# Performance work log

Measured on AMD Instinct MI355X. Metric: run time of the kernel, lower is better.

The kernel has to match this reference:

```python
import jax, jax.numpy as jnp
import numpy as np


def setup_inputs() -> dict:
    key = jax.random.key(0)
    ks = jax.random.split(key, 8)
    B, S, F, K, E, N = 20000, 10, 128, 16, 128, 200000
    nodes = jax.random.randint(ks[0], (B,), 0, N)
    neigh_idx = jax.random.randint(ks[1], (B, S), 0, N)
    self_table = jax.random.normal(ks[2], (N, F), dtype=jnp.float32)
    neigh_table = jax.random.normal(ks[3], (N, F), dtype=jnp.float32)
    center = jax.random.normal(ks[4], (K, F), dtype=jnp.float32)
    cluster_mask = jax.random.uniform(ks[5], (K, F), dtype=jnp.float32)
    # xavier-like scaling keeps exp(relu(.)) in a sane range
    weight = jax.random.normal(ks[6], (E, 2 * F), dtype=jnp.float32) * 0.05
    alpha = jax.random.normal(ks[7], (2 * F, 1), dtype=jnp.float32) * 0.05
    return {"nodes": nodes, "neigh_idx": neigh_idx, "self_table": self_table,
            "neigh_table": neigh_table, "center": center, "cluster_mask": cluster_mask,
            "weight": weight, "alpha": alpha}


def reference(nodes, neigh_idx, self_table, neigh_table, center, cluster_mask, weight, alpha):
    B, S = neigh_idx.shape
    F = self_table.shape[1]
    self_feat = self_table[nodes]                       # (B, F)
    neigh = neigh_table[neigh_idx]                      # (B, S, F) gather (== mask.matmul in original)
    # attention over sampled neighbors: exp(relu([self || neigh] @ alpha))
    a_self, a_neigh = alpha[:F, 0], alpha[F:, 0]        # split cat-matmul
    logits = self_feat @ a_self                         # (B,)
    logits = logits[:, None] + neigh @ a_neigh          # (B, S)
    att = jnp.exp(jax.nn.relu(logits))
    att_norm = att / jnp.sum(att, axis=1, keepdims=True)
    # inverse-distance soft assignment to k centers (Student-t, degree 1)
    n2 = jnp.sum(neigh * neigh, axis=-1)                # (B, S)
    c2 = jnp.sum(center * center, axis=-1)              # (K,)
    cross = jnp.einsum('bsf,kf->bsk', neigh, center)    # (B, S, K)
    q = 1.0 / (n2[:, :, None] - 2.0 * cross + c2[None, None, :] + 1.0)  # (B, S, K)
    # clustered features: sum_k q[b,s,k] * mask[k,f] * neigh[b,s,f]
    clustered = neigh * jnp.einsum('bsk,kf->bsf', q, cluster_mask)      # (B, S, F)
    neigh_agg = jnp.sum(clustered * att_norm[:, :, None], axis=1)       # (B, F)
    combined = jnp.concatenate([self_feat, neigh_agg], axis=1)          # (B, 2F)
    return jax.nn.relu(combined @ weight.T)                             # (B, E)
```

## Files before the change

kernel.cpp:

```cpp
#include <hip/hip_runtime.h>
#include <hip/hip_bf16.h>

typedef unsigned short ushort_t;
typedef __attribute__((ext_vector_type(4))) float v4f;
typedef __attribute__((ext_vector_type(8))) short v8s;

#define FDIM 128
#define KCLUST 16
#define CSTRIDE 264

__device__ __forceinline__ ushort_t f2bf(float x) {
    unsigned int u = __float_as_uint(x);
    unsigned int r = (u + 0x7fffu + ((u >> 16) & 1u)) >> 16;
    return (ushort_t)r;
}

__device__ __forceinline__ float wave_reduce_sum(float v) {
    #pragma unroll
    for (int off = 32; off > 0; off >>= 1) v += __shfl_xor(v, off, 64);
    return v;
}

__global__ void pack_weight(const float* __restrict__ W, ushort_t* __restrict__ Wb,
                            long total, long valid) {
    long i = ((long)blockIdx.x * blockDim.x + threadIdx.x) * 4;
    if (i >= total) return;
    float4 v;
    if (i < valid) v = *(const float4*)(W + i);
    else           v = make_float4(0.f, 0.f, 0.f, 0.f);
    ushort_t* dst = Wb + i;
    dst[0] = f2bf(v.x); dst[1] = f2bf(v.y); dst[2] = f2bf(v.z); dst[3] = f2bf(v.w);
}

__global__ __launch_bounds__(256) void fused_agg(
    const int* __restrict__ nodes, const int* __restrict__ neigh_idx,
    const float* __restrict__ self_table, const float* __restrict__ neigh_table,
    const float* __restrict__ center, const float* __restrict__ cluster_mask,
    const float* __restrict__ alpha, const ushort_t* __restrict__ Wb,
    float* __restrict__ out, int B, int S, int E) {

    __shared__ __align__(16) ushort_t comb[16 * CSTRIDE];
    __shared__ __align__(16) float nbuf[4 * 144];
    __shared__ __align__(16) float qbuf[4 * 16];

    int t = threadIdx.x;
    int lane = t & 63, wave = t >> 6;
    int l16 = lane & 15, quad = lane >> 4;

    for (int i = t; i < (12 * CSTRIDE) / 2; i += 256)
        ((unsigned*)(comb + 4 * CSTRIDE))[i] = 0u;

    float as0 = alpha[lane],       as1 = alpha[lane + 64];
    float an0 = alpha[128 + lane], an1 = alpha[192 + lane];

    float cc[32];
    {
        const float* cb = center + l16 * FDIM + quad * 32;
        #pragma unroll
        for (int j = 0; j < 32; j += 4) {
            float4 v = *(const float4*)(cb + j);
            cc[j] = v.x; cc[j+1] = v.y; cc[j+2] = v.z; cc[j+3] = v.w;
        }
    }
    float mk0[KCLUST], mk1[KCLUST];
    #pragma unroll
    for (int kk = 0; kk < KCLUST; kk++) {
        mk0[kk] = cluster_mask[kk * FDIM + lane];
        mk1[kk] = cluster_mask[kk * FDIM + 64 + lane];
    }

    int b0 = blockIdx.x * 4;
    int b = b0 + wave;
    float* nb = nbuf + wave * 144;
    float* qb = qbuf + wave * 16;
    ushort_t* crow = comb + wave * CSTRIDE;

    if (b < B) {
        size_t node = (size_t)nodes[b];
        float s0 = self_table[node * FDIM + lane];
        float s1 = self_table[node * FDIM + 64 + lane];
        float ls = wave_reduce_sum(s0 * as0 + s1 * as1);

        float acc0 = 0.f, acc1 = 0.f, attsum = 0.f;
        const int* nidx = neigh_idx + (size_t)b * S;
        size_t g = (size_t)nidx[0];
        float n0 = neigh_table[g * FDIM + lane];
        float n1 = neigh_table[g * FDIM + 64 + lane];
        for (int s = 0; s < S; s++) {
            float cn0 = n0, cn1 = n1;
            if (s + 1 < S) {
                g = (size_t)nidx[s + 1];
                n0 = neigh_table[g * FDIM + lane];
                n1 = neigh_table[g * FDIM + 64 + lane];
            }
            float ln = wave_reduce_sum(cn0 * an0 + cn1 * an1);
            float att = __expf(fmaxf(ls + ln, 0.f));
            nb[lane + (lane >> 5) * 4] = cn0;
            int f2 = lane + 64;
            nb[f2 + (f2 >> 5) * 4] = cn1;
            float d = 0.f;
            const float* nbb = nb + quad * 36;
            #pragma unroll
            for (int i = 0; i < 8; i++) {
                float4 f4 = *(const float4*)(nbb + i * 4);
                float t0 = f4.x - cc[i*4+0]; d = fmaf(t0, t0, d);
                float t1 = f4.y - cc[i*4+1]; d = fmaf(t1, t1, d);
                float t2 = f4.z - cc[i*4+2]; d = fmaf(t2, t2, d);
                float t3 = f4.w - cc[i*4+3]; d = fmaf(t3, t3, d);
            }
            d += __shfl_xor(d, 16, 64);
            d += __shfl_xor(d, 32, 64);
            float q = __fdividef(att, d + 1.0f);
            if (lane < 16) qb[lane] = q;
            float4 q0 = *(const float4*)(qb + 0);
            float4 q1 = *(const float4*)(qb + 4);
            float4 q2 = *(const float4*)(qb + 8);
            float4 q3 = *(const float4*)(qb + 12);
            float m0, m1;
            m0  = q0.x*mk0[0]  + q0.y*mk0[1]  + q0.z*mk0[2]  + q0.w*mk0[3];
            m0 += q1.x*mk0[4]  + q1.y*mk0[5]  + q1.z*mk0[6]  + q1.w*mk0[7];
            m0 += q2.x*mk0[8]  + q2.y*mk0[9]  + q2.z*mk0[10] + q2.w*mk0[11];
            m0 += q3.x*mk0[12] + q3.y*mk0[13] + q3.z*mk0[14] + q3.w*mk0[15];
            m1  = q0.x*mk1[0]  + q0.y*mk1[1]  + q0.z*mk1[2]  + q0.w*mk1[3];
            m1 += q1.x*mk1[4]  + q1.y*mk1[5]  + q1.z*mk1[6]  + q1.w*mk1[7];
            m1 += q2.x*mk1[8]  + q2.y*mk1[9]  + q2.z*mk1[10] + q2.w*mk1[11];
            m1 += q3.x*mk1[12] + q3.y*mk1[13] + q3.z*mk1[14] + q3.w*mk1[15];
            acc0 += cn0 * m0;
            acc1 += cn1 * m1;
            attsum += att;
        }
        float inv = __fdividef(1.0f, attsum);
        crow[lane]       = f2bf(s0);
        crow[lane + 64]  = f2bf(s1);
        crow[lane + 128] = f2bf(acc0 * inv);
        crow[lane + 192] = f2bf(acc1 * inv);
    } else {
        crow[lane] = 0; crow[lane + 64] = 0;
        crow[lane + 128] = 0; crow[lane + 192] = 0;
    }
    __syncthreads();

    v8s afr[8];
    #pragma unroll
    for (int kk = 0; kk < 8; kk++)
        afr[kk] = *(const v8s*)(comb + l16 * CSTRIDE + kk * 32 + quad * 8);

    int Ntiles = (E + 15) >> 4;
    for (int nt = wave; nt < Ntiles; nt += 4) {
        const ushort_t* wrow = Wb + ((size_t)(nt * 16 + l16)) * 256 + quad * 8;
        v4f acc = {0.f, 0.f, 0.f, 0.f};
        #pragma unroll
        for (int kk = 0; kk < 8; kk++) {
            v8s bfr = *(const v8s*)(wrow + kk * 32);
            acc = __builtin_amdgcn_mfma_f32_16x16x32_bf16(afr[kk], bfr, acc, 0, 0, 0);
        }
        int gcol = nt * 16 + l16;
        if (gcol < E) {
            #pragma unroll
            for (int rr = 0; rr < 4; rr++) {
                int r16 = quad * 4 + rr;
                if (r16 < 4) {
                    int grow = b0 + r16;
                    if (grow < B)
                        out[(size_t)grow * E + gcol] = fmaxf(acc[rr], 0.f);
                }
            }
        }
    }
}

extern "C" void kernel_launch(void* const* d_in, const int* in_sizes, int n_in,
                              void* d_out, int out_size, void* d_ws, size_t ws_size,
                              hipStream_t stream) {
    const int*   nodes        = (const int*)d_in[0];
    const int*   neigh_idx    = (const int*)d_in[1];
    const float* self_table   = (const float*)d_in[2];
    const float* neigh_table  = (const float*)d_in[3];
    const float* center       = (const float*)d_in[4];
    const float* cluster_mask = (const float*)d_in[5];
    const float* weight       = (const float*)d_in[6];
    const float* alpha        = (const float*)d_in[7];
    float* out = (float*)d_out;

    int B = in_sizes[0];
    int S = in_sizes[1] / B;
    int E = in_sizes[6] / (2 * FDIM);

    int Np = ((E + 15) / 16) * 16;
    ushort_t* Wb = (ushort_t*)d_ws;

    long totalW = (long)Np * 256;
    long validW = (long)E * 256;
    int blksW = (int)((totalW + 1023) / 1024);
    pack_weight<<<blksW, 256, 0, stream>>>(weight, Wb, totalW, validW);

    int nblk = (B + 3) / 4;
    fused_agg<<<nblk, 256, 0, stream>>>(
        nodes, neigh_idx, self_table, neigh_table, center, cluster_mask, alpha,
        Wb, out, B, S, E);
}
```

Before: 285.2 us.

## Compute neighbor attention, distances and cluster mixing with bf16 MFMA per wave

Each wave now stages its 10 neighbor rows as bf16 in shared memory, zero-padded to 16. It then uses MFMA to compute the neighbor-center cross terms, the neighbor norms and the attention logits, and a second MFMA pass to multiply the soft-assignment matrix by the transposed cluster mask. This replaces the serial per-neighbor loop of wave reductions and scalar FMAs. The cost is bf16 rounding inside the distance and attention math (norm minus cross terms can lose precision), more shared memory and a per-block setup of converted center and mask tables.

```diff
diff --git a/kernel.cpp b/kernel.cpp
--- a/kernel.cpp
+++ b/kernel.cpp
@@ -8,6 +8,8 @@
 #define FDIM 128
 #define KCLUST 16
 #define CSTRIDE 264
+#define NSTRIDE 136
+#define QSTRIDE 40
 
 __device__ __forceinline__ ushort_t f2bf(float x) {
     unsigned int u = __float_as_uint(x);
@@ -40,110 +42,152 @@
     float* __restrict__ out, int B, int S, int E) {
 
     __shared__ __align__(16) ushort_t comb[16 * CSTRIDE];
-    __shared__ __align__(16) float nbuf[4 * 144];
-    __shared__ __align__(16) float qbuf[4 * 16];
+    __shared__ __align__(16) ushort_t nrow[4][16 * NSTRIDE];
+    __shared__ __align__(16) ushort_t cenB[16 * NSTRIDE];
+    __shared__ __align__(16) ushort_t maskT[FDIM * QSTRIDE];
+    __shared__ __align__(16) ushort_t aB[FDIM];
+    __shared__ __align__(16) ushort_t qmat[4][16 * QSTRIDE];
+    __shared__ __align__(16) float    n2w[4][16];
+    __shared__ __align__(16) float    c2s[KCLUST];
 
     int t = threadIdx.x;
     int lane = t & 63, wave = t >> 6;
     int l16 = lane & 15, quad = lane >> 4;
 
+    for (int i = t; i < KCLUST * FDIM; i += 256) {
+        int k = i >> 7, f = i & 127;
+        cenB[k * NSTRIDE + f] = f2bf(center[i]);
+        maskT[f * QSTRIDE + k] = f2bf(cluster_mask[i]);
+    }
+    for (int i = t; i < FDIM * 12; i += 256) {
+        int f = i / 12, c = i - f * 12;
+        ((unsigned*)maskT)[f * (QSTRIDE / 2) + 8 + c] = 0u;
+    }
+    if (t < FDIM) aB[t] = f2bf(alpha[128 + t]);
+    if (t < KCLUST) {
+        const float4* cp = (const float4*)(center + t * FDIM);
+        float acc = 0.f;
+        #pragma unroll
+        for (int j = 0; j < 32; j++) {
+            float4 v = cp[j];
+            acc += v.x * v.x + v.y * v.y + v.z * v.z + v.w * v.w;
+        }
+        c2s[t] = acc;
+    }
     for (int i = t; i < (12 * CSTRIDE) / 2; i += 256)
         ((unsigned*)(comb + 4 * CSTRIDE))[i] = 0u;
-
-    float as0 = alpha[lane],       as1 = alpha[lane + 64];
-    float an0 = alpha[128 + lane], an1 = alpha[192 + lane];
-
-    float cc[32];
     {
-        const float* cb = center + l16 * FDIM + quad * 32;
-        #pragma unroll
-        for (int j = 0; j < 32; j += 4) {
-            float4 v = *(const float4*)(cb + j);
-            cc[j] = v.x; cc[j+1] = v.y; cc[j+2] = v.z; cc[j+3] = v.w;
-        }
-    }
-    float mk0[KCLUST], mk1[KCLUST];
-    #pragma unroll
-    for (int kk = 0; kk < KCLUST; kk++) {
-        mk0[kk] = cluster_mask[kk * FDIM + lane];
-        mk1[kk] = cluster_mask[kk * FDIM + 64 + lane];
+        unsigned* qz = (unsigned*)(qmat[wave]);
+        #pragma unroll
+        for (int j = 0; j < 2; j++) {
+            int d = lane + 64 * j;
+            int r = d >> 3, c = d & 7;
+            qz[r * (QSTRIDE / 2) + 8 + c] = 0u;
+        }
     }
 
     int b0 = blockIdx.x * 4;
     int b = b0 + wave;
-    float* nb = nbuf + wave * 144;
-    float* qb = qbuf + wave * 16;
+    ushort_t* nr = nrow[wave];
+    ushort_t* qm = qmat[wave];
+    float* n2p = n2w[wave];
     ushort_t* crow = comb + wave * CSTRIDE;
 
+    float ls = 0.f;
     if (b < B) {
         size_t node = (size_t)nodes[b];
         float s0 = self_table[node * FDIM + lane];
         float s1 = self_table[node * FDIM + 64 + lane];
-        float ls = wave_reduce_sum(s0 * as0 + s1 * as1);
-
-        float acc0 = 0.f, acc1 = 0.f, attsum = 0.f;
+        float as0 = alpha[lane], as1 = alpha[lane + 64];
+        ls = wave_reduce_sum(s0 * as0 + s1 * as1);
+        crow[lane] = f2bf(s0);
+        crow[64 + lane] = f2bf(s1);
         const int* nidx = neigh_idx + (size_t)b * S;
-        size_t g = (size_t)nidx[0];
-        float n0 = neigh_table[g * FDIM + lane];
-        float n1 = neigh_table[g * FDIM + 64 + lane];
         for (int s = 0; s < S; s++) {
-            float cn0 = n0, cn1 = n1;
-            if (s + 1 < S) {
-                g = (size_t)nidx[s + 1];
-                n0 = neigh_table[g * FDIM + lane];
-                n1 = neigh_table[g * FDIM + 64 + lane];
-            }
-            float ln = wave_reduce_sum(cn0 * an0 + cn1 * an1);
-            float att = __expf(fmaxf(ls + ln, 0.f));
-            nb[lane + (lane >> 5) * 4] = cn0;
-            int f2 = lane + 64;
-            nb[f2 + (f2 >> 5) * 4] = cn1;
-            float d = 0.f;
-            const float* nbb = nb + quad * 36;
-            #pragma unroll
-            for (int i = 0; i < 8; i++) {
-                float4 f4 = *(const float4*)(nbb + i * 4);
-                float t0 = f4.x - cc[i*4+0]; d = fmaf(t0, t0, d);
-                float t1 = f4.y - cc[i*4+1]; d = fmaf(t1, t1, d);
-                float t2 = f4.z - cc[i*4+2]; d = fmaf(t2, t2, d);
-                float t3 = f4.w - cc[i*4+3]; d = fmaf(t3, t3, d);
-            }
-            d += __shfl_xor(d, 16, 64);
-            d += __shfl_xor(d, 32, 64);
-            float q = __fdividef(att, d + 1.0f);
-            if (lane < 16) qb[lane] = q;
-            float4 q0 = *(const float4*)(qb + 0);
-            float4 q1 = *(const float4*)(qb + 4);
-            float4 q2 = *(const float4*)(qb + 8);
-            float4 q3 = *(const float4*)(qb + 12);
-            float m0, m1;
-            m0  = q0.x*mk0[0]  + q0.y*mk0[1]  + q0.z*mk0[2]  + q0.w*mk0[3];
-            m0 += q1.x*mk0[4]  + q1.y*mk0[5]  + q1.z*mk0[6]  + q1.w*mk0[7];
-            m0 += q2.x*mk0[8]  + q2.y*mk0[9]  + q2.z*mk0[10] + q2.w*mk0[11];
-            m0 += q3.x*mk0[12] + q3.y*mk0[13] + q3.z*mk0[14] + q3.w*mk0[15];
-            m1  = q0.x*mk1[0]  + q0.y*mk1[1]  + q0.z*mk1[2]  + q0.w*mk1[3];
-            m1 += q1.x*mk1[4]  + q1.y*mk1[5]  + q1.z*mk1[6]  + q1.w*mk1[7];
-            m1 += q2.x*mk1[8]  + q2.y*mk1[9]  + q2.z*mk1[10] + q2.w*mk1[11];
-            m1 += q3.x*mk1[12] + q3.y*mk1[13] + q3.z*mk1[14] + q3.w*mk1[15];
-            acc0 += cn0 * m0;
-            acc1 += cn1 * m1;
-            attsum += att;
-        }
-        float inv = __fdividef(1.0f, attsum);
-        crow[lane]       = f2bf(s0);
-        crow[lane + 64]  = f2bf(s1);
-        crow[lane + 128] = f2bf(acc0 * inv);
-        crow[lane + 192] = f2bf(acc1 * inv);
+            size_t g = (size_t)nidx[s];
+            float2 v = *(const float2*)(neigh_table + g * FDIM + 2 * lane);
+            unsigned pk = ((unsigned)f2bf(v.y) << 16) | (unsigned)f2bf(v.x);
+            *(unsigned*)(nr + s * NSTRIDE + 2 * lane) = pk;
+        }
+        for (int s = S; s < 16; s++)
+            *(unsigned*)(nr + s * NSTRIDE + 2 * lane) = 0u;
     } else {
-        crow[lane] = 0; crow[lane + 64] = 0;
-        crow[lane + 128] = 0; crow[lane + 192] = 0;
-    }
+        for (int s = 0; s < 16; s++)
+            *(unsigned*)(nr + s * NSTRIDE + 2 * lane) = 0u;
+        crow[lane] = 0; crow[64 + lane] = 0;
+    }
+
     __syncthreads();
 
-    v8s afr[8];
+    v8s afr[4], cfr[4], abf[4];
+    #pragma unroll
+    for (int kk = 0; kk < 4; kk++) {
+        afr[kk] = *(const v8s*)(nr + l16 * NSTRIDE + kk * 32 + quad * 8);
+        cfr[kk] = *(const v8s*)(cenB + l16 * NSTRIDE + kk * 32 + quad * 8);
+        abf[kk] = *(const v8s*)(aB + kk * 32 + quad * 8);
+    }
+    v4f cracc = {0.f, 0.f, 0.f, 0.f};
+    v4f nnacc = {0.f, 0.f, 0.f, 0.f};
+    v4f lnacc = {0.f, 0.f, 0.f, 0.f};
+    #pragma unroll
+    for (int kk = 0; kk < 4; kk++) {
+        cracc = __builtin_amdgcn_mfma_f32_16x16x32_bf16(afr[kk], cfr[kk], cracc, 0, 0, 0);
+        nnacc = __builtin_amdgcn_mfma_f32_16x16x32_bf16(afr[kk], afr[kk], nnacc, 0, 0, 0);
+        lnacc = __builtin_amdgcn_mfma_f32_16x16x32_bf16(afr[kk], abf[kk], lnacc, 0, 0, 0);
+    }
+    if (quad == (l16 >> 2)) {
+        int r = l16 & 3;
+        float dv = (r == 0) ? nnacc[0] : (r == 1) ? nnacc[1] : (r == 2) ? nnacc[2] : nnacc[3];
+        n2p[l16] = dv;
+    }
+    float c2l = c2s[l16];
+    float4 n2q = *(const float4*)(n2p + quad * 4);
+
+    float asum = 0.f, qv[4];
+    #pragma unroll
+    for (int r = 0; r < 4; r++) {
+        int s = quad * 4 + r;
+        float att = (s < S) ? __expf(fmaxf(ls + lnacc[r], 0.f)) : 0.f;
+        asum += att;
+        float d = n2q[r] - 2.f * cracc[r] + c2l + 1.f;
+        qv[r] = __fdividef(att, d);
+    }
+    asum += __shfl_xor(asum, 16, 64);
+    asum += __shfl_xor(asum, 32, 64);
+    float inv = __fdividef(1.f, asum);
+    #pragma unroll
+    for (int r = 0; r < 4; r++)
+        qm[(quad * 4 + r) * QSTRIDE + l16] = f2bf(qv[r]);
+
+    v8s qfr = *(const v8s*)(qm + l16 * QSTRIDE + quad * 8);
+    v4f macc[8];
+    #pragma unroll
+    for (int fb = 0; fb < 8; fb++) {
+        v8s mfr = *(const v8s*)(maskT + (fb * 16 + l16) * QSTRIDE + quad * 8);
+        v4f z = {0.f, 0.f, 0.f, 0.f};
+        macc[fb] = __builtin_amdgcn_mfma_f32_16x16x32_bf16(qfr, mfr, z, 0, 0, 0);
+    }
+    #pragma unroll
+    for (int fb = 0; fb < 8; fb++) {
+        float tacc = 0.f;
+        #pragma unroll
+        for (int r = 0; r < 4; r++) {
+            int s = quad * 4 + r;
+            ushort_t nv = nr[s * NSTRIDE + fb * 16 + l16];
+            float nf = __uint_as_float((unsigned)nv << 16);
+            tacc = fmaf(macc[fb][r], nf, tacc);
+        }
+        tacc += __shfl_xor(tacc, 16, 64);
+        tacc += __shfl_xor(tacc, 32, 64);
+        if ((fb & 3) == quad)
+            crow[128 + fb * 16 + l16] = f2bf(tacc * inv);
+    }
+    __syncthreads();
+
+    v8s bafr[8];
     #pragma unroll
     for (int kk = 0; kk < 8; kk++)
-        afr[kk] = *(const v8s*)(comb + l16 * CSTRIDE + kk * 32 + quad * 8);
+        bafr[kk] = *(const v8s*)(comb + l16 * CSTRIDE + kk * 32 + quad * 8);
 
     int Ntiles = (E + 15) >> 4;
     for (int nt = wave; nt < Ntiles; nt += 4) {
@@ -152,7 +196,7 @@
         #pragma unroll
         for (int kk = 0; kk < 8; kk++) {
             v8s bfr = *(const v8s*)(wrow + kk * 32);
-            acc = __builtin_amdgcn_mfma_f32_16x16x32_bf16(afr[kk], bfr, acc, 0, 0, 0);
+            acc = __builtin_amdgcn_mfma_f32_16x16x32_bf16(bafr[kk], bfr, acc, 0, 0, 0);
         }
         int gcol = nt * 16 + l16;
         if (gcol < E) {
```

New measurement: 290.0 us. No clear change (+1.7%).
